# Optimization experiments

Measured on AMD Instinct MI355X. Metric: run time of the kernel, lower is better.

The kernel has to match this reference:

```python
import jax, jax.numpy as jnp
import numpy as np

N_PART = 22
N_DIM = 3
H0 = 8
H_SIZE = H0 + 1  # + time condition
HID = 64
N_LAYERS = 4
B = 1024


def _base_edges(n):
    rows, cols = [], []
    for i in range(n):
        for j in range(i + 1, n):
            rows += [i, j]
            cols += [j, i]
    return np.asarray(rows, np.int32), np.asarray(cols, np.int32)


def _batched_edges(n_batch, n_nodes):
    r0, c0 = _base_edges(n_nodes)
    offs = (np.arange(n_batch, dtype=np.int32) * n_nodes)[:, None]
    rows = (r0[None, :] + offs).reshape(-1)
    cols = (c0[None, :] + offs).reshape(-1)
    return jnp.asarray(rows), jnp.asarray(cols)


def setup_inputs() -> dict:
    key = jax.random.key(0)
    ks = jax.random.split(key, 24)
    s = 0.1
    L = N_LAYERS
    d = {
        't': jax.random.uniform(ks[0], (B, 1), jnp.float32),
        'xs': jax.random.normal(ks[1], (B, N_PART * N_DIM), jnp.float32),
        'h_initial': jax.random.normal(ks[2], (N_PART, H0), jnp.float32),
        'emb_w': jax.random.normal(ks[3], (H_SIZE, HID), jnp.float32) * s,
        'emb_b': jnp.zeros((HID,), jnp.float32),
        'emb_out_w': jax.random.normal(ks[4], (HID, H_SIZE), jnp.float32) * s,
        'emb_out_b': jnp.zeros((H_SIZE,), jnp.float32),
        # edge_mlp: in = 2*HID + 1 (radial) + 1 (edge_attr) = 130
        'edge_w1': jax.random.normal(ks[5], (L, 2 * HID + 2, HID), jnp.float32) * s,
        'edge_b1': jnp.zeros((L, HID), jnp.float32),
        'edge_w2': jax.random.normal(ks[6], (L, HID, HID), jnp.float32) * s,
        'edge_b2': jnp.zeros((L, HID), jnp.float32),
        # node_mlp: in = HID (h) + HID (agg) = 128
        'node_w1': jax.random.normal(ks[7], (L, 2 * HID, HID), jnp.float32) * s,
        'node_b1': jnp.zeros((L, HID), jnp.float32),
        'node_w2': jax.random.normal(ks[8], (L, HID, HID), jnp.float32) * s,
        'node_b2': jnp.zeros((L, HID), jnp.float32),
        # coord_mlp: Lin(HID,HID) -> SiLU -> Lin(HID,1, no bias, xavier gain 0.001)
        'coord_w1': jax.random.normal(ks[9], (L, HID, HID), jnp.float32) * s,
        'coord_b1': jnp.zeros((L, HID), jnp.float32),
        'coord_w2': jax.random.normal(ks[10], (L, HID, 1), jnp.float32) * 0.001,
    }
    return d


def _egnn_forward(t, xs, h_initial, emb_w, emb_b, emb_out_w, emb_out_b,
                  edge_w1, edge_b1, edge_w2, edge_b2,
                  node_w1, node_b1, node_w2, node_b2,
                  coord_w1, coord_b1, coord_w2, rows, cols):
    silu = jax.nn.silu
    n_batch = xs.shape[0]
    N = n_batch * N_PART
    x0 = xs[:, :N_PART * N_DIM].reshape(N, N_DIM)

    # node features: atom features tiled over batch + time column
    h = jnp.tile(h_initial[None], (n_batch, 1, 1)).reshape(N, H0)
    t_nodes = jnp.repeat(t.reshape(n_batch, 1), N_PART, axis=0)  # (N,1)
    h = jnp.concatenate([h, t_nodes], axis=-1)  # (N, H_SIZE)

    # static edge attribute: squared distance at input coords
    d0 = x0[rows] - x0[cols]
    edge_attr = jnp.sum(d0 * d0, axis=-1, keepdims=True)  # (E,1)

    h = h @ emb_w + emb_b  # embedding
    x = x0
    for i in range(N_LAYERS):
        diff = x[rows] - x[cols]                       # (E,3)
        radial = jnp.sum(diff * diff, -1, keepdims=True)
        diff = diff / jnp.sqrt(radial + 1e-8)          # norm_diff=True
        ef = jnp.concatenate([h[rows], h[cols], radial, edge_attr], -1)
        m = silu(ef @ edge_w1[i] + edge_b1[i])
        m = silu(m @ edge_w2[i] + edge_b2[i])          # edge messages (E,HID)
        # equivariant coordinate update (tanh=False)
        scal = silu(m @ coord_w1[i] + coord_b1[i]) @ coord_w2[i]  # (E,1)
        x = x + jax.ops.segment_sum(diff * scal, rows, num_segments=N)
        # node update with residual (recurrent=True)
        agg = jax.ops.segment_sum(m, rows, num_segments=N)
        hn = silu(jnp.concatenate([h, agg], -1) @ node_w1[i] + node_b1[i])
        h = h + (hn @ node_w2[i] + node_b2[i])
    _ = h @ emb_out_w + emb_out_b  # embedding_out (h output unused by EGNN_AD2_CV)

    vel = (x - x0).reshape(n_batch, N_PART, N_DIM)
    vel = vel - jnp.mean(vel, axis=1, keepdims=True)   # remove_mean
    return vel.reshape(n_batch, N_PART * N_DIM)


def reference(t, xs, h_initial, emb_w, emb_b, emb_out_w, emb_out_b,
              edge_w1, edge_b1, edge_w2, edge_b2,
              node_w1, node_b1, node_w2, node_b2,
              coord_w1, coord_b1, coord_w2):
    rows, cols = _batched_edges(xs.shape[0], N_PART)
    return _egnn_forward(t, xs, h_initial, emb_w, emb_b, emb_out_w, emb_out_b,
                         edge_w1, edge_b1, edge_w2, edge_b2,
                         node_w1, node_b1, node_w2, node_b2,
                         coord_w1, coord_b1, coord_w2, rows, cols)
```

## Files before the change

### kernel.cpp

```cpp
#include <hip/hip_runtime.h>
#include <hip/hip_fp16.h>

#define NPART 22
#define NDEG  21
#define NEDGE 462
#define HID   64
#define NLAYERS 4
#define NSTRIPB 29
#define MW2S  72

typedef _Float16 f16x8 __attribute__((ext_vector_type(8)));
typedef __attribute__((ext_vector_type(4))) float f32x4;
typedef __attribute__((ext_vector_type(4))) unsigned int u32x4;

__device__ __forceinline__ float silu_f(float v) {
    return __fdividef(v, 1.0f + __expf(-v));
}
__device__ __forceinline__ unsigned short hfu(float v) {
    return __half_as_ushort(__float2half(v));
}

__global__ void prep_wfrag(const float* __restrict__ edge_w2,
                           const float* __restrict__ coord_w1,
                           unsigned* __restrict__ wfrag)
{
    const int m = blockIdx.x;
    const int l = threadIdx.x;
    const int L = m >> 1;
    const float* W = (m & 1) ? (coord_w1 + L*HID*HID) : (edge_w2 + L*HID*HID);
    const int kg = l >> 4, j0 = l & 15;
    u32x4* ws4 = (u32x4*)wfrag;
    #pragma unroll
    for (int nt = 0; nt < 4; ++nt) {
        #pragma unroll
        for (int c = 0; c < 2; ++c) {
            u32x4 p;
            #pragma unroll
            for (int pi = 0; pi < 4; ++pi) {
                int k = c*32 + kg*8 + 2*pi;
                float v0 = W[k*HID + nt*16 + j0];
                float v1 = W[(k+1)*HID + nt*16 + j0];
                p[pi] = (unsigned)hfu(v0) | ((unsigned)hfu(v1) << 16);
            }
            ws4[m*512 + (nt*2 + c)*64 + l] = p;
        }
    }
}

__global__ void prep_nfrag(const float* __restrict__ node_w1,
                           const float* __restrict__ node_w2,
                           const float* __restrict__ edge_w1,
                           unsigned* __restrict__ nfrag)
{
    const int b = blockIdx.x;
    const int L = b >> 2, mat = b & 3;
    const int l = threadIdx.x;
    const int kg = l >> 4, j0 = l & 15;
    u32x4* nf = (u32x4*)nfrag + (size_t)L*40*64;
    const float* W; int nc, base;
    if      (mat == 0) { W = node_w1 + L*2*HID*HID;            nc = 4; base = 0;  }
    else if (mat == 1) { W = node_w2 + L*HID*HID;              nc = 2; base = 16; }
    else if (mat == 2) { W = edge_w1 + (L+1)*130*HID;          nc = 2; base = 24; }
    else               { W = edge_w1 + (L+1)*130*HID + 64*HID; nc = 2; base = 32; }
    for (int nt = 0; nt < 4; ++nt) {
        for (int c = 0; c < nc; ++c) {
            u32x4 p;
            #pragma unroll
            for (int pi = 0; pi < 4; ++pi) {
                int k = c*32 + kg*8 + 2*pi;
                float v0 = W[k*HID + nt*16 + j0];
                float v1 = W[(k+1)*HID + nt*16 + j0];
                p[pi] = (unsigned)hfu(v0) | ((unsigned)hfu(v1) << 16);
            }
            nf[(size_t)(base + nt*nc + c)*64 + l] = p;
        }
    }
}

__global__ __launch_bounds__(256, 4)
void k_init(const float* __restrict__ t_in, const float* __restrict__ xs,
            const float* __restrict__ h_init,
            const float* __restrict__ emb_w, const float* __restrict__ emb_b,
            const float* __restrict__ edge_w1, const float* __restrict__ edge_b1,
            float* __restrict__ xw, float* __restrict__ hw,
            float* __restrict__ Hrw, float* __restrict__ Hcw, int NT)
{
    __shared__ __align__(16) float hbuf[4][68];
    const int w = threadIdx.x >> 6, l = threadIdx.x & 63;
    const int n = blockIdx.x*4 + w;
    if (n >= NT) return;
    const int bidx = n / NPART, p = n - bidx*NPART;
    float hv = emb_b[l] + t_in[bidx]*emb_w[8*HID + l];
    #pragma unroll
    for (int k = 0; k < 8; ++k) hv += h_init[p*8 + k]*emb_w[k*HID + l];
    hw[(size_t)n*HID + l] = hv;
    hbuf[w][l] = hv;
    float accr = edge_b1[l], accc = 0.f;
    #pragma unroll 4
    for (int k = 0; k < HID; ++k) {
        float hk = hbuf[w][k];
        accr += hk*edge_w1[k*HID + l];
        accc += hk*edge_w1[(HID + k)*HID + l];
    }
    Hrw[(size_t)n*HID + l] = accr;
    Hcw[(size_t)n*HID + l] = accc;
    if (l < 3) xw[n*3 + l] = xs[n*3 + l];
}

__global__ __launch_bounds__(256, 4)
void k_edgeA(const float* __restrict__ edge_w1v,
             const float* __restrict__ edge_b2L,
             const float* __restrict__ coord_b1L,
             const float* __restrict__ coord_w2L,
             const unsigned* __restrict__ wfrag,
             const float* __restrict__ xs,
             const float* __restrict__ xw,
             const float* __restrict__ Hrw,
             const float* __restrict__ Hcw,
             float* __restrict__ aggpart,
             float* __restrict__ scalg,
             int nstrips, int Lmat)
{
    __shared__ __align__(16) unsigned short mwall[4][16*MW2S];
    __shared__ __align__(16) float xst[4][2][68];

    const int tid = threadIdx.x, l = tid & 63, w = tid >> 6;
    const int kg = l >> 4, j0 = l & 15;

    const int sid = blockIdx.x*4 + w;
    if (sid >= nstrips) return;
    const int batch = sid / NSTRIPB, s = sid - batch*NSTRIPB;
    const int e0 = s*16;
    const int ecnt = (NEDGE - e0 < 16) ? (NEDGE - e0) : 16;
    const int n0 = e0 / NDEG;

    {
        const int base = batch*(NPART*3);
        xst[w][0][l] = xw[base + l];
        xst[w][1][l] = xs[base + l];
        if (l < 2) { xst[w][0][64+l] = xw[base+64+l]; xst[w][1][64+l] = xs[base+64+l]; }
    }

    int eg = e0 + j0; if (eg >= NEDGE) eg = NEDGE - 1;
    const int a  = eg / NDEG;
    const int r  = eg - a*NDEG;
    const int bb = r + (r >= a ? 1 : 0);
    float d0 = xst[w][0][a*3+0] - xst[w][0][bb*3+0];
    float d1 = xst[w][0][a*3+1] - xst[w][0][bb*3+1];
    float d2 = xst[w][0][a*3+2] - xst[w][0][bb*3+2];
    float rad = d0*d0 + d1*d1 + d2*d2;
    float g0 = xst[w][1][a*3+0] - xst[w][1][bb*3+0];
    float g1 = xst[w][1][a*3+1] - xst[w][1][bb*3+1];
    float g2 = xst[w][1][a*3+2] - xst[w][1][bb*3+2];
    float eav = g0*g0 + g1*g1 + g2*g2;

    const u32x4* ws4 = (const u32x4*)wfrag;
    const u32x4* wb1 = ws4 + (size_t)(Lmat*2    )*512 + l;
    const u32x4* wb2 = ws4 + (size_t)(Lmat*2 + 1)*512 + l;
    f16x8 BW1[4][2];
    #pragma unroll
    for (int nt = 0; nt < 4; ++nt) {
        BW1[nt][0] = __builtin_bit_cast(f16x8, wb1[(nt*2 + 0)*64]);
        BW1[nt][1] = __builtin_bit_cast(f16x8, wb1[(nt*2 + 1)*64]);
    }

    f16x8 A1[2];
    {
        const float* hrp = Hrw + (size_t)(batch*NPART + a)*HID;
        const float* hcp = Hcw + (size_t)(batch*NPART + bb)*HID;
        #pragma unroll
        for (int c = 0; c < 2; ++c) {
            const int k0 = c*32 + kg*8;
            float4 ra = *(const float4*)(hrp + k0);
            float4 rb = *(const float4*)(hrp + k0 + 4);
            float4 ca = *(const float4*)(hcp + k0);
            float4 cb = *(const float4*)(hcp + k0 + 4);
            float4 va = *(const float4*)(edge_w1v + k0);
            float4 vb = *(const float4*)(edge_w1v + k0 + 4);
            float4 ua = *(const float4*)(edge_w1v + 64 + k0);
            float4 ub = *(const float4*)(edge_w1v + 64 + k0 + 4);
            f16x8 A;
            A[0] = (_Float16)silu_f(ra.x + ca.x + rad*va.x + eav*ua.x);
            A[1] = (_Float16)silu_f(ra.y + ca.y + rad*va.y + eav*ua.y);
            A[2] = (_Float16)silu_f(ra.z + ca.z + rad*va.z + eav*ua.z);
            A[3] = (_Float16)silu_f(ra.w + ca.w + rad*va.w + eav*ua.w);
            A[4] = (_Float16)silu_f(rb.x + cb.x + rad*vb.x + eav*ub.x);
            A[5] = (_Float16)silu_f(rb.y + cb.y + rad*vb.y + eav*ub.y);
            A[6] = (_Float16)silu_f(rb.z + cb.z + rad*vb.z + eav*ub.z);
            A[7] = (_Float16)silu_f(rb.w + cb.w + rad*vb.w + eav*ub.w);
            A1[c] = A;
        }
    }

    f32x4 acc[4];
    #pragma unroll
    for (int nt = 0; nt < 4; ++nt) {
        f32x4 z = {0.f, 0.f, 0.f, 0.f};
        z = __builtin_amdgcn_mfma_f32_16x16x32_f16(A1[0], BW1[nt][0], z, 0, 0, 0);
        z = __builtin_amdgcn_mfma_f32_16x16x32_f16(A1[1], BW1[nt][1], z, 0, 0, 0);
        acc[nt] = z;
    }

    f16x8 B2[4][2];
    #pragma unroll
    for (int nt = 0; nt < 4; ++nt) {
        B2[nt][0] = __builtin_bit_cast(f16x8, wb2[(nt*2 + 0)*64]);
        B2[nt][1] = __builtin_bit_cast(f16x8, wb2[(nt*2 + 1)*64]);
    }

    int sel[4], emask[4];
    #pragma unroll
    for (int r2 = 0; r2 < 4; ++r2) {
        int e2 = kg*4 + r2;
        int eg2 = e0 + e2; if (eg2 >= NEDGE) eg2 = NEDGE - 1;
        sel[r2] = (eg2 / NDEG == n0);
        emask[r2] = (e2 < ecnt);
    }
    unsigned short* mw = mwall[w];
    float pS[4] = {0.f,0.f,0.f,0.f}, pT[4] = {0.f,0.f,0.f,0.f};
    #pragma unroll
    for (int nt = 0; nt < 4; ++nt) {
        int j = nt*16 + j0;
        float bv = edge_b2L[j];
        #pragma unroll
        for (int r2 = 0; r2 < 4; ++r2) {
            float mv = emask[r2] ? silu_f(acc[nt][r2] + bv) : 0.f;
            mw[(kg*4 + r2)*MW2S + j] = hfu(mv);
            pT[nt] += mv;
            pS[nt] += sel[r2] ? mv : 0.f;
        }
    }
    #pragma unroll
    for (int nt = 0; nt < 4; ++nt) {
        pS[nt] += __shfl_xor(pS[nt], 16);
        pS[nt] += __shfl_xor(pS[nt], 32);
        pT[nt] += __shfl_xor(pT[nt], 16);
        pT[nt] += __shfl_xor(pT[nt], 32);
    }
    {
        float* apb = aggpart + (size_t)(batch*NSTRIPB + s)*128;
        if (kg == 0) {
            #pragma unroll
            for (int nt = 0; nt < 4; ++nt) apb[nt*16 + j0] = pS[nt];
        } else if (kg == 1) {
            #pragma unroll
            for (int nt = 0; nt < 4; ++nt) apb[64 + nt*16 + j0] = pT[nt] - pS[nt];
        }
    }

    f16x8 A2[2];
    {
        const unsigned short* arp = mw + j0*MW2S;
        A2[0] = *(const f16x8*)(arp + kg*8);
        A2[1] = *(const f16x8*)(arp + 32 + kg*8);
    }

    f32x4 acc2[4];
    #pragma unroll
    for (int nt = 0; nt < 4; ++nt) {
        f32x4 z = {0.f, 0.f, 0.f, 0.f};
        z = __builtin_amdgcn_mfma_f32_16x16x32_f16(A2[0], B2[nt][0], z, 0, 0, 0);
        z = __builtin_amdgcn_mfma_f32_16x16x32_f16(A2[1], B2[nt][1], z, 0, 0, 0);
        acc2[nt] = z;
    }

    float pr[4] = {0.f,0.f,0.f,0.f};
    #pragma unroll
    for (int nt = 0; nt < 4; ++nt) {
        int j = nt*16 + j0;
        float cb = coord_b1L[j], cw = coord_w2L[j];
        #pragma unroll
        for (int r2 = 0; r2 < 4; ++r2)
            pr[r2] += silu_f(acc2[nt][r2] + cb) * cw;
    }
    #pragma unroll
    for (int off = 8; off > 0; off >>= 1) {
        #pragma unroll
        for (int r2 = 0; r2 < 4; ++r2)
            pr[r2] += __shfl_xor(pr[r2], off);
    }
    if (j0 == 0) {
        #pragma unroll
        for (int r2 = 0; r2 < 4; ++r2) {
            int e2 = kg*4 + r2;
            if (e2 < ecnt) scalg[(size_t)batch*464 + e0 + e2] = pr[r2];
        }
    }
}

__global__ __launch_bounds__(256, 2)
void k_dxnode(const float* __restrict__ scalg, float* __restrict__ xw, int NB, int gD,
              const unsigned* __restrict__ nfragL,
              const float* __restrict__ nb1p, const float* __restrict__ nb2p,
              const float* __restrict__ eb1p,
              const float* __restrict__ aggpart,
              float* __restrict__ hw,
              float* __restrict__ Hrw, float* __restrict__ Hcw,
              int NT, int nstripN)
{
    __shared__ __align__(16) float hT[4][16][68];
    __shared__ __align__(16) float hnT[4][16][68];
    __shared__ float xstd[4][68], dxd[4][68];
    const int tid = threadIdx.x, l = tid & 63, w = tid >> 6;
    const int kg = l >> 4, j0 = l & 15;

    if (blockIdx.x < (unsigned)gD) {
        const int batch = blockIdx.x*4 + w;
        if (batch >= NB) return;
        xstd[w][l] = xw[batch*66 + ((l < 66) ? l : 0)];
        if (l < 2) xstd[w][64 + l] = xw[batch*66 + 64 + l];
        dxd[w][l] = 0.f;
        if (l < 4) dxd[w][64 + l] = 0.f;
        for (int e = l; e < NEDGE; e += 64) {
            int a = e / NDEG, r = e - a*NDEG;
            int bb = r + (r >= a ? 1 : 0);
            float d0 = xstd[w][a*3+0] - xstd[w][bb*3+0];
            float d1 = xstd[w][a*3+1] - xstd[w][bb*3+1];
            float d2 = xstd[w][a*3+2] - xstd[w][bb*3+2];
            float inv = rsqrtf(d0*d0 + d1*d1 + d2*d2 + 1e-8f);
            float sc = scalg[(size_t)batch*464 + e] * inv;
            atomicAdd(&dxd[w][a*3+0], d0*sc);
            atomicAdd(&dxd[w][a*3+1], d1*sc);
            atomicAdd(&dxd[w][a*3+2], d2*sc);
        }
        xw[batch*66 + ((l < 66) ? l : 0)] = xstd[w][l] + dxd[w][l];
        if (l < 2) xw[batch*66 + 64 + l] = xstd[w][64 + l] + dxd[w][64 + l];
        return;
    }

    const int sid = (blockIdx.x - gD)*4 + w;
    if (sid >= nstripN) return;

    {
        int row = l >> 2, cc = (l & 3) << 4;
        int nd = sid*16 + row; if (nd >= NT) nd = NT - 1;
        const float* src = hw + (size_t)nd*HID + cc;
        *(float4*)&hT[w][row][cc]      = *(const float4*)(src);
        *(float4*)&hT[w][row][cc + 4]  = *(const float4*)(src + 4);
        *(float4*)&hT[w][row][cc + 8]  = *(const float4*)(src + 8);
        *(float4*)&hT[w][row][cc + 12] = *(const float4*)(src + 12);
    }

    const int ndl  = sid*16 + j0;
    const int ndc  = (ndl < NT) ? ndl : NT - 1;
    const int bidx = ndc / NPART, p = ndc - bidx*NPART;

    f16x8 A1[4];
    #pragma unroll
    for (int c = 0; c < 2; ++c) {
        f16x8 A;
        #pragma unroll
        for (int i = 0; i < 8; ++i) A[i] = (_Float16)hT[w][j0][c*32 + kg*8 + i];
        A1[c] = A;
    }
    {
        const int smin = (NDEG*p) >> 4;
        const int smax = (NDEG*p + 20) >> 4;
        #pragma unroll
        for (int c = 2; c < 4; ++c) {
            const int k0a = (c - 2)*32 + kg*8;
            float tv[8] = {0.f,0.f,0.f,0.f,0.f,0.f,0.f,0.f};
            for (int s = smin; s <= smax; ++s) {
                int slot = (p == (s*16)/NDEG) ? 0 : 1;
                const float* ap = aggpart + (size_t)(bidx*NSTRIPB + s)*128 + slot*64 + k0a;
                float4 qa = *(const float4*)ap;
                float4 qb = *(const float4*)(ap + 4);
                tv[0] += qa.x; tv[1] += qa.y; tv[2] += qa.z; tv[3] += qa.w;
                tv[4] += qb.x; tv[5] += qb.y; tv[6] += qb.z; tv[7] += qb.w;
            }
            f16x8 A;
            #pragma unroll
            for (int i = 0; i < 8; ++i) A[i] = (_Float16)tv[i];
            A1[c] = A;
        }
    }

    const u32x4* nf = (const u32x4*)nfragL;
    #define NBF(idx) __builtin_bit_cast(f16x8, nf[(size_t)(idx)*64 + l])

    f32x4 acc1[4];
    #pragma unroll
    for (int nt = 0; nt < 4; ++nt) {
        f32x4 z = {0.f, 0.f, 0.f, 0.f};
        #pragma unroll
        for (int c = 0; c < 4; ++c)
            z = __builtin_amdgcn_mfma_f32_16x16x32_f16(A1[c], NBF(nt*4 + c), z, 0, 0, 0);
        acc1[nt] = z;
    }
    #pragma unroll
    for (int nt = 0; nt < 4; ++nt) {
        float bv = nb1p[nt*16 + j0];
        #pragma unroll
        for (int r2 = 0; r2 < 4; ++r2)
            hnT[w][kg*4 + r2][nt*16 + j0] = silu_f(acc1[nt][r2] + bv);
    }

    f16x8 A2[2];
    #pragma unroll
    for (int c = 0; c < 2; ++c) {
        f16x8 A;
        #pragma unroll
        for (int i = 0; i < 8; ++i) A[i] = (_Float16)hnT[w][j0][c*32 + kg*8 + i];
        A2[c] = A;
    }
    f32x4 acc2[4];
    #pragma unroll
    for (int nt = 0; nt < 4; ++nt) {
        f32x4 z = {0.f, 0.f, 0.f, 0.f};
        #pragma unroll
        for (int c = 0; c < 2; ++c)
            z = __builtin_amdgcn_mfma_f32_16x16x32_f16(A2[c], NBF(16 + nt*2 + c), z, 0, 0, 0);
        acc2[nt] = z;
    }
    #pragma unroll
    for (int nt = 0; nt < 4; ++nt) {
        float bv = nb2p[nt*16 + j0];
        #pragma unroll
        for (int r2 = 0; r2 < 4; ++r2) {
            int row = kg*4 + r2, col = nt*16 + j0;
            float hv = hT[w][row][col] + acc2[nt][r2] + bv;
            hnT[w][row][col] = hv;
            int nd = sid*16 + row;
            if (nd < NT) hw[(size_t)nd*HID + col] = hv;
        }
    }

    f16x8 A3[2];
    #pragma unroll
    for (int c = 0; c < 2; ++c) {
        f16x8 A;
        #pragma unroll
        for (int i = 0; i < 8; ++i) A[i] = (_Float16)hnT[w][j0][c*32 + kg*8 + i];
        A3[c] = A;
    }
    f32x4 accR[4], accC[4];
    #pragma unroll
    for (int nt = 0; nt < 4; ++nt) {
        f32x4 zr = {0.f,0.f,0.f,0.f}, zc = {0.f,0.f,0.f,0.f};
        #pragma unroll
        for (int c = 0; c < 2; ++c) {
            zr = __builtin_amdgcn_mfma_f32_16x16x32_f16(A3[c], NBF(24 + nt*2 + c), zr, 0, 0, 0);
            zc = __builtin_amdgcn_mfma_f32_16x16x32_f16(A3[c], NBF(32 + nt*2 + c), zc, 0, 0, 0);
        }
        accR[nt] = zr; accC[nt] = zc;
    }
    #pragma unroll
    for (int nt = 0; nt < 4; ++nt) {
        float bv = eb1p[nt*16 + j0];
        #pragma unroll
        for (int r2 = 0; r2 < 4; ++r2) {
            int row = kg*4 + r2, col = nt*16 + j0;
            int nd = sid*16 + row;
            if (nd < NT) {
                Hrw[(size_t)nd*HID + col] = accR[nt][r2] + bv;
                Hcw[(size_t)nd*HID + col] = accC[nt][r2];
            }
        }
    }
    #undef NBF
}

__global__ void k_final(const float* __restrict__ xw, const float* __restrict__ xs,
                        const float* __restrict__ scalg, float* __restrict__ out)
{
    __shared__ float xstB[68], dxB[68], vb[68], mv3[3];
    const int b = blockIdx.x, t = threadIdx.x;
    if (t < 66) xstB[t] = xw[b*66 + t];
    if (t < 68) dxB[t] = 0.f;
    __syncthreads();
    for (int e = t; e < NEDGE; e += 256) {
        int a = e / NDEG, r = e - a*NDEG;
        int bb = r + (r >= a ? 1 : 0);
        float d0 = xstB[a*3+0] - xstB[bb*3+0];
        float d1 = xstB[a*3+1] - xstB[bb*3+1];
        float d2 = xstB[a*3+2] - xstB[bb*3+2];
        float inv = rsqrtf(d0*d0 + d1*d1 + d2*d2 + 1e-8f);
        float sc = scalg[(size_t)b*464 + e] * inv;
        atomicAdd(&dxB[a*3+0], d0*sc);
        atomicAdd(&dxB[a*3+1], d1*sc);
        atomicAdd(&dxB[a*3+2], d2*sc);
    }
    __syncthreads();
    if (t < 66) vb[t] = xstB[t] + dxB[t] - xs[b*66 + t];
    __syncthreads();
    if (t < 3) {
        float s = 0.f;
        #pragma unroll
        for (int p = 0; p < NPART; ++p) s += vb[p*3 + t];
        mv3[t] = s / (float)NPART;
    }
    __syncthreads();
    if (t < 66) out[b*66 + t] = vb[t] - mv3[t % 3];
}

extern "C" void kernel_launch(void* const* d_in, const int* in_sizes, int n_in,
                              void* d_out, int out_size, void* d_ws, size_t ws_size,
                              hipStream_t stream) {
    const float* t_in     = (const float*)d_in[0];
    const float* xs       = (const float*)d_in[1];
    const float* h_init   = (const float*)d_in[2];
    const float* emb_w    = (const float*)d_in[3];
    const float* emb_b    = (const float*)d_in[4];
    const float* edge_w1  = (const float*)d_in[7];
    const float* edge_b1  = (const float*)d_in[8];
    const float* edge_w2  = (const float*)d_in[9];
    const float* edge_b2  = (const float*)d_in[10];
    const float* node_w1  = (const float*)d_in[11];
    const float* node_b1  = (const float*)d_in[12];
    const float* node_w2  = (const float*)d_in[13];
    const float* node_b2  = (const float*)d_in[14];
    const float* coord_w1 = (const float*)d_in[15];
    const float* coord_b1 = (const float*)d_in[16];
    const float* coord_w2 = (const float*)d_in[17];
    float* outp = (float*)d_out;

    const int NB = in_sizes[0];
    const int NT = NB * NPART;
    float* xw      = (float*)d_ws;
    float* hw      = xw   + (size_t)NT*3;
    float* Hrw     = hw   + (size_t)NT*HID;
    float* Hcw     = Hrw  + (size_t)NT*HID;
    float* aggpart = Hcw  + (size_t)NT*HID;
    float* scalg   = aggpart + (size_t)NB*NSTRIPB*128;
    unsigned* wfrag = (unsigned*)(scalg + (size_t)NB*464);
    unsigned* nfrag = wfrag + (size_t)8*512*4;

    const int nstrips = NB * NSTRIPB;
    const int gA = (nstrips + 3) / 4;
    const int gI = (NT + 3) / 4;
    const int nstripN = (NT + 15) / 16;
    const int gN = (nstripN + 3) / 4;
    const int gD = (NB + 3) / 4;

    prep_wfrag<<<8, 64, 0, stream>>>(edge_w2, coord_w1, wfrag);
    prep_nfrag<<<12, 64, 0, stream>>>(node_w1, node_w2, edge_w1, nfrag);
    k_init<<<gI, 256, 0, stream>>>(t_in, xs, h_init, emb_w, emb_b,
                                   edge_w1, edge_b1, xw, hw, Hrw, Hcw, NT);
    for (int L = 0; L < NLAYERS; ++L) {
        k_edgeA<<<gA, 256, 0, stream>>>(
            edge_w1 + L*130*HID + 128*HID,
            edge_b2 + L*HID, coord_b1 + L*HID, coord_w2 + L*HID,
            wfrag, xs, xw, Hrw, Hcw, aggpart, scalg, nstrips, L);
        if (L < NLAYERS - 1) {
            k_dxnode<<<gD + gN, 256, 0, stream>>>(
                scalg, xw, NB, gD,
                nfrag + (size_t)L*40*64*4,
                node_b1 + L*HID, node_b2 + L*HID, edge_b1 + (L+1)*HID,
                aggpart, hw, Hrw, Hcw, NT, nstripN);
        }
    }
    k_final<<<NB, 256, 0, stream>>>(xw, xs, scalg, outp);
}
```

Baseline: 354.8 us.

## Process two edge strips per wave and precompute static edge attributes

Each wave in the edge kernel now handles a pair of 16-edge strips. The weight fragments, biases and coordinate tile are loaded once and reused across both strips. The squared distances on the original coordinates (edge_attr) do not change across layers, so a new one-time kernel computes them into a workspace buffer and the edge kernel reads them instead of recomputing. This halves the wave count and the redundant weight loads per layer, at the cost of less parallelism and more serial work per wave.

```diff
diff --git a/kernel.cpp b/kernel.cpp
--- a/kernel.cpp
+++ b/kernel.cpp
@@ -7,6 +7,7 @@
 #define HID   64
 #define NLAYERS 4
 #define NSTRIPB 29
+#define NPAIRB  15
 #define MW2S  72
 
 typedef _Float16 f16x8 __attribute__((ext_vector_type(8)));
@@ -77,6 +78,22 @@
     }
 }
 
+__global__ void k_eav(const float* __restrict__ xs, float* __restrict__ eavg)
+{
+    __shared__ float xsh[68];
+    const int b = blockIdx.x, t = threadIdx.x;
+    if (t < 66) xsh[t] = xs[b*66 + t];
+    __syncthreads();
+    for (int e = t; e < NEDGE; e += 256) {
+        int a = e / NDEG, r = e - a*NDEG;
+        int bb = r + (r >= a ? 1 : 0);
+        float d0 = xsh[a*3+0] - xsh[bb*3+0];
+        float d1 = xsh[a*3+1] - xsh[bb*3+1];
+        float d2 = xsh[a*3+2] - xsh[bb*3+2];
+        eavg[(size_t)b*464 + e] = d0*d0 + d1*d1 + d2*d2;
+    }
+}
+
 __global__ __launch_bounds__(256, 4)
 void k_init(const float* __restrict__ t_in, const float* __restrict__ xs,
             const float* __restrict__ h_init,
@@ -113,177 +130,178 @@
              const float* __restrict__ coord_b1L,
              const float* __restrict__ coord_w2L,
              const unsigned* __restrict__ wfrag,
-             const float* __restrict__ xs,
+             const float* __restrict__ eavg,
              const float* __restrict__ xw,
              const float* __restrict__ Hrw,
              const float* __restrict__ Hcw,
              float* __restrict__ aggpart,
              float* __restrict__ scalg,
-             int nstrips, int Lmat)
+             int npairs, int Lmat)
 {
     __shared__ __align__(16) unsigned short mwall[4][16*MW2S];
-    __shared__ __align__(16) float xst[4][2][68];
+    __shared__ __align__(16) float xst[4][68];
 
     const int tid = threadIdx.x, l = tid & 63, w = tid >> 6;
     const int kg = l >> 4, j0 = l & 15;
 
-    const int sid = blockIdx.x*4 + w;
-    if (sid >= nstrips) return;
-    const int batch = sid / NSTRIPB, s = sid - batch*NSTRIPB;
-    const int e0 = s*16;
-    const int ecnt = (NEDGE - e0 < 16) ? (NEDGE - e0) : 16;
-    const int n0 = e0 / NDEG;
+    const int pid = blockIdx.x*4 + w;
+    if (pid >= npairs) return;
+    const int batch = pid / NPAIRB, t = pid - batch*NPAIRB;
 
     {
-        const int base = batch*(NPART*3);
-        xst[w][0][l] = xw[base + l];
-        xst[w][1][l] = xs[base + l];
-        if (l < 2) { xst[w][0][64+l] = xw[base+64+l]; xst[w][1][64+l] = xs[base+64+l]; }
-    }
-
-    int eg = e0 + j0; if (eg >= NEDGE) eg = NEDGE - 1;
-    const int a  = eg / NDEG;
-    const int r  = eg - a*NDEG;
-    const int bb = r + (r >= a ? 1 : 0);
-    float d0 = xst[w][0][a*3+0] - xst[w][0][bb*3+0];
-    float d1 = xst[w][0][a*3+1] - xst[w][0][bb*3+1];
-    float d2 = xst[w][0][a*3+2] - xst[w][0][bb*3+2];
-    float rad = d0*d0 + d1*d1 + d2*d2;
-    float g0 = xst[w][1][a*3+0] - xst[w][1][bb*3+0];
-    float g1 = xst[w][1][a*3+1] - xst[w][1][bb*3+1];
-    float g2 = xst[w][1][a*3+2] - xst[w][1][bb*3+2];
-    float eav = g0*g0 + g1*g1 + g2*g2;
+        const int base = batch*66;
+        xst[w][l] = xw[base + ((l < 66) ? l : 0)];
+        if (l < 2) xst[w][64 + l] = xw[base + 64 + l];
+    }
 
     const u32x4* ws4 = (const u32x4*)wfrag;
     const u32x4* wb1 = ws4 + (size_t)(Lmat*2    )*512 + l;
     const u32x4* wb2 = ws4 + (size_t)(Lmat*2 + 1)*512 + l;
-    f16x8 BW1[4][2];
+    f16x8 BW1[4][2], B2[4][2];
     #pragma unroll
     for (int nt = 0; nt < 4; ++nt) {
         BW1[nt][0] = __builtin_bit_cast(f16x8, wb1[(nt*2 + 0)*64]);
         BW1[nt][1] = __builtin_bit_cast(f16x8, wb1[(nt*2 + 1)*64]);
-    }
-
-    f16x8 A1[2];
-    {
-        const float* hrp = Hrw + (size_t)(batch*NPART + a)*HID;
-        const float* hcp = Hcw + (size_t)(batch*NPART + bb)*HID;
-        #pragma unroll
-        for (int c = 0; c < 2; ++c) {
-            const int k0 = c*32 + kg*8;
-            float4 ra = *(const float4*)(hrp + k0);
-            float4 rb = *(const float4*)(hrp + k0 + 4);
-            float4 ca = *(const float4*)(hcp + k0);
-            float4 cb = *(const float4*)(hcp + k0 + 4);
-            float4 va = *(const float4*)(edge_w1v + k0);
-            float4 vb = *(const float4*)(edge_w1v + k0 + 4);
-            float4 ua = *(const float4*)(edge_w1v + 64 + k0);
-            float4 ub = *(const float4*)(edge_w1v + 64 + k0 + 4);
-            f16x8 A;
-            A[0] = (_Float16)silu_f(ra.x + ca.x + rad*va.x + eav*ua.x);
-            A[1] = (_Float16)silu_f(ra.y + ca.y + rad*va.y + eav*ua.y);
-            A[2] = (_Float16)silu_f(ra.z + ca.z + rad*va.z + eav*ua.z);
-            A[3] = (_Float16)silu_f(ra.w + ca.w + rad*va.w + eav*ua.w);
-            A[4] = (_Float16)silu_f(rb.x + cb.x + rad*vb.x + eav*ub.x);
-            A[5] = (_Float16)silu_f(rb.y + cb.y + rad*vb.y + eav*ub.y);
-            A[6] = (_Float16)silu_f(rb.z + cb.z + rad*vb.z + eav*ub.z);
-            A[7] = (_Float16)silu_f(rb.w + cb.w + rad*vb.w + eav*ub.w);
-            A1[c] = A;
-        }
-    }
-
-    f32x4 acc[4];
-    #pragma unroll
-    for (int nt = 0; nt < 4; ++nt) {
-        f32x4 z = {0.f, 0.f, 0.f, 0.f};
-        z = __builtin_amdgcn_mfma_f32_16x16x32_f16(A1[0], BW1[nt][0], z, 0, 0, 0);
-        z = __builtin_amdgcn_mfma_f32_16x16x32_f16(A1[1], BW1[nt][1], z, 0, 0, 0);
-        acc[nt] = z;
-    }
-
-    f16x8 B2[4][2];
-    #pragma unroll
-    for (int nt = 0; nt < 4; ++nt) {
-        B2[nt][0] = __builtin_bit_cast(f16x8, wb2[(nt*2 + 0)*64]);
-        B2[nt][1] = __builtin_bit_cast(f16x8, wb2[(nt*2 + 1)*64]);
-    }
-
-    int sel[4], emask[4];
-    #pragma unroll
-    for (int r2 = 0; r2 < 4; ++r2) {
-        int e2 = kg*4 + r2;
-        int eg2 = e0 + e2; if (eg2 >= NEDGE) eg2 = NEDGE - 1;
-        sel[r2] = (eg2 / NDEG == n0);
-        emask[r2] = (e2 < ecnt);
-    }
+        B2[nt][0]  = __builtin_bit_cast(f16x8, wb2[(nt*2 + 0)*64]);
+        B2[nt][1]  = __builtin_bit_cast(f16x8, wb2[(nt*2 + 1)*64]);
+    }
+    float bv[4], cb[4], cw[4];
+    #pragma unroll
+    for (int nt = 0; nt < 4; ++nt) {
+        bv[nt] = edge_b2L[nt*16 + j0];
+        cb[nt] = coord_b1L[nt*16 + j0];
+        cw[nt] = coord_w2L[nt*16 + j0];
+    }
+
     unsigned short* mw = mwall[w];
-    float pS[4] = {0.f,0.f,0.f,0.f}, pT[4] = {0.f,0.f,0.f,0.f};
-    #pragma unroll
-    for (int nt = 0; nt < 4; ++nt) {
-        int j = nt*16 + j0;
-        float bv = edge_b2L[j];
-        #pragma unroll
-        for (int r2 = 0; r2 < 4; ++r2) {
-            float mv = emask[r2] ? silu_f(acc[nt][r2] + bv) : 0.f;
-            mw[(kg*4 + r2)*MW2S + j] = hfu(mv);
-            pT[nt] += mv;
-            pS[nt] += sel[r2] ? mv : 0.f;
-        }
-    }
-    #pragma unroll
-    for (int nt = 0; nt < 4; ++nt) {
-        pS[nt] += __shfl_xor(pS[nt], 16);
-        pS[nt] += __shfl_xor(pS[nt], 32);
-        pT[nt] += __shfl_xor(pT[nt], 16);
-        pT[nt] += __shfl_xor(pT[nt], 32);
-    }
-    {
-        float* apb = aggpart + (size_t)(batch*NSTRIPB + s)*128;
-        if (kg == 0) {
-            #pragma unroll
-            for (int nt = 0; nt < 4; ++nt) apb[nt*16 + j0] = pS[nt];
-        } else if (kg == 1) {
-            #pragma unroll
-            for (int nt = 0; nt < 4; ++nt) apb[64 + nt*16 + j0] = pT[nt] - pS[nt];
-        }
-    }
-
-    f16x8 A2[2];
-    {
-        const unsigned short* arp = mw + j0*MW2S;
-        A2[0] = *(const f16x8*)(arp + kg*8);
-        A2[1] = *(const f16x8*)(arp + 32 + kg*8);
-    }
-
-    f32x4 acc2[4];
-    #pragma unroll
-    for (int nt = 0; nt < 4; ++nt) {
-        f32x4 z = {0.f, 0.f, 0.f, 0.f};
-        z = __builtin_amdgcn_mfma_f32_16x16x32_f16(A2[0], B2[nt][0], z, 0, 0, 0);
-        z = __builtin_amdgcn_mfma_f32_16x16x32_f16(A2[1], B2[nt][1], z, 0, 0, 0);
-        acc2[nt] = z;
-    }
-
-    float pr[4] = {0.f,0.f,0.f,0.f};
-    #pragma unroll
-    for (int nt = 0; nt < 4; ++nt) {
-        int j = nt*16 + j0;
-        float cb = coord_b1L[j], cw = coord_w2L[j];
-        #pragma unroll
-        for (int r2 = 0; r2 < 4; ++r2)
-            pr[r2] += silu_f(acc2[nt][r2] + cb) * cw;
-    }
-    #pragma unroll
-    for (int off = 8; off > 0; off >>= 1) {
-        #pragma unroll
-        for (int r2 = 0; r2 < 4; ++r2)
-            pr[r2] += __shfl_xor(pr[r2], off);
-    }
-    if (j0 == 0) {
+
+    for (int half = 0; half < 2; ++half) {
+        const int s = 2*t + half;
+        if (s >= NSTRIPB) break;
+        const int e0 = s*16;
+        const int ecnt = (NEDGE - e0 < 16) ? (NEDGE - e0) : 16;
+        const int n0 = e0 / NDEG;
+
+        int eg = e0 + j0; if (eg >= NEDGE) eg = NEDGE - 1;
+        const int a  = eg / NDEG;
+        const int r  = eg - a*NDEG;
+        const int bb = r + (r >= a ? 1 : 0);
+        float d0 = xst[w][a*3+0] - xst[w][bb*3+0];
+        float d1 = xst[w][a*3+1] - xst[w][bb*3+1];
+        float d2 = xst[w][a*3+2] - xst[w][bb*3+2];
+        float rad = d0*d0 + d1*d1 + d2*d2;
+        float eav = eavg[(size_t)batch*464 + eg];
+
+        f16x8 A1[2];
+        {
+            const float* hrp = Hrw + (size_t)(batch*NPART + a)*HID;
+            const float* hcp = Hcw + (size_t)(batch*NPART + bb)*HID;
+            #pragma unroll
+            for (int c = 0; c < 2; ++c) {
+                const int k0 = c*32 + kg*8;
+                float4 ra = *(const float4*)(hrp + k0);
+                float4 rb = *(const float4*)(hrp + k0 + 4);
+                float4 ca = *(const float4*)(hcp + k0);
+                float4 cb4 = *(const float4*)(hcp + k0 + 4);
+                float4 va = *(const float4*)(edge_w1v + k0);
+                float4 vb = *(const float4*)(edge_w1v + k0 + 4);
+                float4 ua = *(const float4*)(edge_w1v + 64 + k0);
+                float4 ub = *(const float4*)(edge_w1v + 64 + k0 + 4);
+                f16x8 A;
+                A[0] = (_Float16)silu_f(ra.x + ca.x + rad*va.x + eav*ua.x);
+                A[1] = (_Float16)silu_f(ra.y + ca.y + rad*va.y + eav*ua.y);
+                A[2] = (_Float16)silu_f(ra.z + ca.z + rad*va.z + eav*ua.z);
+                A[3] = (_Float16)silu_f(ra.w + ca.w + rad*va.w + eav*ua.w);
+                A[4] = (_Float16)silu_f(rb.x + cb4.x + rad*vb.x + eav*ub.x);
+                A[5] = (_Float16)silu_f(rb.y + cb4.y + rad*vb.y + eav*ub.y);
+                A[6] = (_Float16)silu_f(rb.z + cb4.z + rad*vb.z + eav*ub.z);
+                A[7] = (_Float16)silu_f(rb.w + cb4.w + rad*vb.w + eav*ub.w);
+                A1[c] = A;
+            }
+        }
+
+        f32x4 acc[4];
+        #pragma unroll
+        for (int nt = 0; nt < 4; ++nt) {
+            f32x4 z = {0.f, 0.f, 0.f, 0.f};
+            z = __builtin_amdgcn_mfma_f32_16x16x32_f16(A1[0], BW1[nt][0], z, 0, 0, 0);
+            z = __builtin_amdgcn_mfma_f32_16x16x32_f16(A1[1], BW1[nt][1], z, 0, 0, 0);
+            acc[nt] = z;
+        }
+
+        int sel[4], emask[4];
         #pragma unroll
         for (int r2 = 0; r2 < 4; ++r2) {
             int e2 = kg*4 + r2;
-            if (e2 < ecnt) scalg[(size_t)batch*464 + e0 + e2] = pr[r2];
+            int eg2 = e0 + e2; if (eg2 >= NEDGE) eg2 = NEDGE - 1;
+            sel[r2] = (eg2 / NDEG == n0);
+            emask[r2] = (e2 < ecnt);
+        }
+        float pS[4] = {0.f,0.f,0.f,0.f}, pT[4] = {0.f,0.f,0.f,0.f};
+        #pragma unroll
+        for (int nt = 0; nt < 4; ++nt) {
+            int j = nt*16 + j0;
+            #pragma unroll
+            for (int r2 = 0; r2 < 4; ++r2) {
+                float mv = emask[r2] ? silu_f(acc[nt][r2] + bv[nt]) : 0.f;
+                mw[(kg*4 + r2)*MW2S + j] = hfu(mv);
+                pT[nt] += mv;
+                pS[nt] += sel[r2] ? mv : 0.f;
+            }
+        }
+        #pragma unroll
+        for (int nt = 0; nt < 4; ++nt) {
+            pS[nt] += __shfl_xor(pS[nt], 16);
+            pS[nt] += __shfl_xor(pS[nt], 32);
+            pT[nt] += __shfl_xor(pT[nt], 16);
+            pT[nt] += __shfl_xor(pT[nt], 32);
+        }
+        {
+            float* apb = aggpart + (size_t)(batch*NSTRIPB + s)*128;
+            if (kg == 0) {
+                #pragma unroll
+                for (int nt = 0; nt < 4; ++nt) apb[nt*16 + j0] = pS[nt];
+            } else if (kg == 1) {
+                #pragma unroll
+                for (int nt = 0; nt < 4; ++nt) apb[64 + nt*16 + j0] = pT[nt] - pS[nt];
+            }
+        }
+
+        f16x8 A2[2];
+        {
+            const unsigned short* arp = mw + j0*MW2S;
+            A2[0] = *(const f16x8*)(arp + kg*8);
+            A2[1] = *(const f16x8*)(arp + 32 + kg*8);
+        }
+
+        f32x4 acc2[4];
+        #pragma unroll
+        for (int nt = 0; nt < 4; ++nt) {
+            f32x4 z = {0.f, 0.f, 0.f, 0.f};
+            z = __builtin_amdgcn_mfma_f32_16x16x32_f16(A2[0], B2[nt][0], z, 0, 0, 0);
+            z = __builtin_amdgcn_mfma_f32_16x16x32_f16(A2[1], B2[nt][1], z, 0, 0, 0);
+            acc2[nt] = z;
+        }
+
+        float pr[4] = {0.f,0.f,0.f,0.f};
+        #pragma unroll
+        for (int nt = 0; nt < 4; ++nt) {
+            #pragma unroll
+            for (int r2 = 0; r2 < 4; ++r2)
+                pr[r2] += silu_f(acc2[nt][r2] + cb[nt]) * cw[nt];
+        }
+        #pragma unroll
+        for (int off = 8; off > 0; off >>= 1) {
+            #pragma unroll
+            for (int r2 = 0; r2 < 4; ++r2)
+                pr[r2] += __shfl_xor(pr[r2], off);
+        }
+        if (j0 == 0) {
+            #pragma unroll
+            for (int r2 = 0; r2 < 4; ++r2) {
+                int e2 = kg*4 + r2;
+                if (e2 < ecnt) scalg[(size_t)batch*464 + e0 + e2] = pr[r2];
+            }
         }
     }
 }
@@ -522,11 +540,12 @@
     float* Hcw     = Hrw  + (size_t)NT*HID;
     float* aggpart = Hcw  + (size_t)NT*HID;
     float* scalg   = aggpart + (size_t)NB*NSTRIPB*128;
-    unsigned* wfrag = (unsigned*)(scalg + (size_t)NB*464);
+    float* eavg    = scalg + (size_t)NB*464;
+    unsigned* wfrag = (unsigned*)(eavg + (size_t)NB*464);
     unsigned* nfrag = wfrag + (size_t)8*512*4;
 
-    const int nstrips = NB * NSTRIPB;
-    const int gA = (nstrips + 3) / 4;
+    const int npairs = NB * NPAIRB;
+    const int gA = (npairs + 3) / 4;
     const int gI = (NT + 3) / 4;
     const int nstripN = (NT + 15) / 16;
     const int gN = (nstripN + 3) / 4;
@@ -534,13 +553,14 @@
 
     prep_wfrag<<<8, 64, 0, stream>>>(edge_w2, coord_w1, wfrag);
     prep_nfrag<<<12, 64, 0, stream>>>(node_w1, node_w2, edge_w1, nfrag);
+    k_eav<<<NB, 256, 0, stream>>>(xs, eavg);
     k_init<<<gI, 256, 0, stream>>>(t_in, xs, h_init, emb_w, emb_b,
                                    edge_w1, edge_b1, xw, hw, Hrw, Hcw, NT);
     for (int L = 0; L < NLAYERS; ++L) {
         k_edgeA<<<gA, 256, 0, stream>>>(
             edge_w1 + L*130*HID + 128*HID,
             edge_b2 + L*HID, coord_b1 + L*HID, coord_w2 + L*HID,
-            wfrag, xs, xw, Hrw, Hcw, aggpart, scalg, nstrips, L);
+            wfrag, eavg, xw, Hrw, Hcw, aggpart, scalg, npairs, L);
         if (L < NLAYERS - 1) {
             k_dxnode<<<gD + gN, 256, 0, stream>>>(
                 scalg, xw, NB, gD,
```

Result: slower. 407.2 us (+14.8%).
